# Performance work log

Measured on AMD Instinct MI355X. Metric: run time of the kernel, lower is better.

## Reference

```python
import jax, jax.numpy as jnp
import numpy as np

WS = 8          # window_size
SHIFT = 4       # shift_size
NUM_HEADS = 8
DIM = 256
HIDDEN = 1024   # mlp_ratio * dim
EPS = 1e-5


def _rel_pos_index(ws):
    # static numpy computation of Swin relative position index, shape (ws*ws, ws*ws)
    coords = np.stack(np.meshgrid(np.arange(ws), np.arange(ws), indexing='ij')).reshape(2, -1)
    rel = coords[:, :, None] - coords[:, None, :]            # (2, N, N)
    rel = rel.transpose(1, 2, 0).astype(np.int64)            # (N, N, 2)
    rel[..., 0] += ws - 1
    rel[..., 1] += ws - 1
    rel[..., 0] *= 2 * ws - 1
    return rel.sum(-1)                                       # (N, N)

_REL_IDX = _rel_pos_index(WS)


def _layer_norm(x, g, b):
    m = jnp.mean(x, axis=-1, keepdims=True)
    v = jnp.mean(jnp.square(x - m), axis=-1, keepdims=True)
    return (x - m) * jax.lax.rsqrt(v + EPS) * g + b


def _window_partition(x, ws):
    B, H, W, C = x.shape
    x = x.reshape(B, H // ws, ws, W // ws, ws, C)
    return x.transpose(0, 1, 3, 2, 4, 5).reshape(-1, ws * ws, C)


def _window_reverse(win, ws, B, H, W):
    C = win.shape[-1]
    x = win.reshape(B, H // ws, W // ws, ws, ws, C)
    return x.transpose(0, 1, 3, 2, 4, 5).reshape(B, H, W, C)


def setup_inputs() -> dict:
    key = jax.random.key(0)
    ks = jax.random.split(key, 16)
    s = 0.02
    inp = {
        'x': jax.random.normal(ks[0], (8, 16384, 256), jnp.float32),
        'norm1_w': jnp.ones((DIM,), jnp.float32),
        'norm1_b': jnp.zeros((DIM,), jnp.float32),
        'qkv_w': jax.random.normal(ks[1], (3 * DIM, DIM), jnp.float32) * s,
        'qkv_b': jnp.zeros((3 * DIM,), jnp.float32),
        'rpb_table': jax.random.normal(ks[2], ((2 * WS - 1) * (2 * WS - 1), NUM_HEADS), jnp.float32) * s,
        'proj_w': jax.random.normal(ks[3], (DIM, DIM), jnp.float32) * s,
        'proj_b': jnp.zeros((DIM,), jnp.float32),
        'norm2_w': jnp.ones((DIM,), jnp.float32),
        'norm2_b': jnp.zeros((DIM,), jnp.float32),
        'fc1_w': jax.random.normal(ks[4], (HIDDEN, DIM), jnp.float32) * s,
        'fc1_b': jnp.zeros((HIDDEN,), jnp.float32),
        'fc2_w': jax.random.normal(ks[5], (DIM, HIDDEN), jnp.float32) * s,
        'fc2_b': jnp.zeros((DIM,), jnp.float32),
        'h': 128,
        'w': 128,
    }
    return inp


def reference(x, norm1_w, norm1_b, qkv_w, qkv_b, rpb_table, proj_w, proj_b,
              norm2_w, norm2_b, fc1_w, fc1_b, fc2_w, fc2_b, h, w):
    B, L, C = x.shape
    H, W = int(h), int(w)
    nh, hd = NUM_HEADS, C // NUM_HEADS
    scale = hd ** -0.5
    N = WS * WS

    shortcut = x
    xn = _layer_norm(x, norm1_w, norm1_b).reshape(B, H, W, C)
    # cyclic shift (SW-MSA)
    xs = jnp.roll(xn, shift=(-SHIFT, -SHIFT), axis=(1, 2))
    xw = _window_partition(xs, WS)                           # (B_, N, C)

    # window attention
    qkv = xw @ qkv_w.T + qkv_b                               # (B_, N, 3C)
    qkv = qkv.reshape(-1, N, 3, nh, hd).transpose(2, 0, 3, 1, 4)
    q, k, v = qkv[0], qkv[1], qkv[2]                         # (B_, nh, N, hd)
    attn = jnp.einsum('bhnd,bhmd->bhnm', q * scale, k)
    bias = rpb_table[_REL_IDX.reshape(-1)].reshape(N, N, nh).transpose(2, 0, 1)
    attn = jax.nn.softmax(attn + bias[None], axis=-1)
    out = jnp.einsum('bhnm,bhmd->bhnd', attn, v)
    out = out.transpose(0, 2, 1, 3).reshape(-1, N, C)
    out = out @ proj_w.T + proj_b

    # merge windows and reverse shift
    xs = _window_reverse(out, WS, B, H, W)
    xo = jnp.roll(xs, shift=(SHIFT, SHIFT), axis=(1, 2)).reshape(B, H * W, C)

    x = shortcut + xo
    # MLP with residual
    y = _layer_norm(x, norm2_w, norm2_b)
    y = jax.nn.gelu(y @ fc1_w.T + fc1_b, approximate=False)
    y = y @ fc2_w.T + fc2_b
    return x + y
```

## Files before the change

### kernel.cpp

```cpp
#include <hip/hip_runtime.h>

typedef __bf16 bf16_t;
typedef __bf16 bf16x4 __attribute__((ext_vector_type(4)));
typedef __bf16 bf16x8 __attribute__((ext_vector_type(8)));
typedef float f32x4 __attribute__((ext_vector_type(4)));

#define QKV_SEG 33554432L

#define GLDS(gp, lp)                                                                   \
  __builtin_amdgcn_global_load_lds((const __attribute__((address_space(1))) void*)(gp), \
                                   (__attribute__((address_space(3))) void*)(lp), 16, 0, 0)
#define BAR __builtin_amdgcn_s_barrier()
#define SCHED0 __builtin_amdgcn_sched_barrier(0)
#define MFMA __builtin_amdgcn_mfma_f32_16x16x32_bf16

__global__ __launch_bounds__(256) void cvt_kernel(const float* __restrict__ src,
                                                  bf16_t* __restrict__ dst) {
  int i = (blockIdx.x * 256 + threadIdx.x) * 4;
  float4 v = *(const float4*)(src + i);
  bf16x4 o;
  o[0] = (bf16_t)v.x; o[1] = (bf16_t)v.y; o[2] = (bf16_t)v.z; o[3] = (bf16_t)v.w;
  *(bf16x4*)(dst + i) = o;
}

__global__ __launch_bounds__(256) void ln_kernel(const float* __restrict__ src,
                                                 const float* __restrict__ gw,
                                                 const float* __restrict__ gb,
                                                 bf16_t* __restrict__ dst,
                                                 int shifted) {
  int lane = threadIdx.x & 63, wv = threadIdx.x >> 6;
  long m = (long)blockIdx.x * 4 + wv;
  long srow;
  if (shifted) {
    long b_ = m >> 6; int tok = (int)(m & 63);
    int bb = (int)(b_ >> 8), win = (int)(b_ & 255);
    int wh = win >> 4, ww = win & 15;
    int ii = tok >> 3, jj = tok & 7;
    int hh = (wh * 8 + ii + 4) & 127, wp = (ww * 8 + jj + 4) & 127;
    srow = ((long)bb << 14) + (hh << 7) + wp;
  } else {
    srow = m;
  }
  float4 v = *(const float4*)(src + srow * 256 + lane * 4);
  float s = v.x + v.y + v.z + v.w;
  float s2 = v.x * v.x + v.y * v.y + v.z * v.z + v.w * v.w;
#pragma unroll
  for (int msk = 1; msk < 64; msk <<= 1) {
    s += __shfl_xor(s, msk);
    s2 += __shfl_xor(s2, msk);
  }
  float mean = s * (1.f / 256.f);
  float var = s2 * (1.f / 256.f) - mean * mean;
  float rs = rsqrtf(var + 1e-5f);
  float4 g4 = *(const float4*)(gw + lane * 4);
  float4 b4 = *(const float4*)(gb + lane * 4);
  bf16x4 o;
  o[0] = (bf16_t)((v.x - mean) * rs * g4.x + b4.x);
  o[1] = (bf16_t)((v.y - mean) * rs * g4.y + b4.y);
  o[2] = (bf16_t)((v.z - mean) * rs * g4.z + b4.z);
  o[3] = (bf16_t)((v.w - mean) * rs * g4.w + b4.w);
  *(bf16x4*)(dst + m * 256 + lane * 4) = o;
}

template <int EPI>
__global__ __launch_bounds__(256) void gemm_kernel(const bf16_t* __restrict__ A,
                                                   const bf16_t* __restrict__ Bw,
                                                   const float* __restrict__ bias, int K,
                                                   bf16_t* __restrict__ out_bf, float* out_f,
                                                   const float* resid) {
  __shared__ __align__(16) bf16_t As[2][8192];
  __shared__ __align__(16) bf16_t Bs[2][8192];
  int tid = threadIdx.x;
  int lane = tid & 63, wv = tid >> 6;
  int wm = wv >> 1, wn = wv & 1;

  int GX = gridDim.x, GY = gridDim.y;
  int flat = blockIdx.x + blockIdx.y * GX;
  int xcd = flat & 7, ii = flat >> 3;
  int iq = ii / GX;
  int by = xcd * (GY >> 3) + iq;
  int bx = ii - iq * GX;
  long m0 = (long)by * 128;
  int n0 = bx * 128;
  int lr = lane & 15, g = lane >> 4;

  int csw = (((lane & 7) ^ (lane >> 3)) << 3);
  const bf16_t* gA = A + (m0 + wv * 32 + (lane >> 3)) * K + csw;
  const bf16_t* gB = Bw + (long)(n0 + wv * 32 + (lane >> 3)) * K + csw;

  f32x4 acc[4][4] = {};

#define STAGE(buf, k0)                                                    \
  do {                                                                    \
    _Pragma("unroll") for (int s = 0; s < 4; ++s) {                       \
      GLDS(gA + (long)s * 8 * K + (k0), As[buf] + wv * 2048 + s * 512);   \
      GLDS(gB + (long)s * 8 * K + (k0), Bs[buf] + wv * 2048 + s * 512);   \
    }                                                                     \
  } while (0)

  int nt = K >> 6;
  STAGE(0, 0);
  for (int t = 0; t < nt; ++t) {
    int tb = t & 1;
    if (t + 1 < nt) {
      STAGE(tb ^ 1, (t + 1) << 6);
      asm volatile("s_waitcnt vmcnt(8)" ::: "memory");
    } else {
      asm volatile("s_waitcnt vmcnt(0)" ::: "memory");
    }
    BAR;
    SCHED0;
#pragma unroll
    for (int kk = 0; kk < 2; ++kk) {
      bf16x8 af[4], bfr[4];
#pragma unroll
      for (int mf = 0; mf < 4; ++mf)
        af[mf] = *(const bf16x8*)(As[tb] + (wm * 64 + mf * 16 + lr) * 64 +
                                  (((kk * 4 + g) ^ (lr & 7)) << 3));
#pragma unroll
      for (int nf = 0; nf < 4; ++nf)
        bfr[nf] = *(const bf16x8*)(Bs[tb] + (wn * 64 + nf * 16 + lr) * 64 +
                                   (((kk * 4 + g) ^ (lr & 7)) << 3));
#pragma unroll
      for (int mf = 0; mf < 4; ++mf)
#pragma unroll
        for (int nf = 0; nf < 4; ++nf)
          acc[mf][nf] = MFMA(af[mf], bfr[nf], acc[mf][nf], 0, 0, 0);
    }
    BAR;
  }
#undef STAGE

#pragma unroll
  for (int mf = 0; mf < 4; ++mf) {
#pragma unroll
    for (int nf = 0; nf < 4; ++nf) {
      long mb = m0 + wm * 64 + mf * 16 + 4 * g;
      int n = n0 + wn * 64 + nf * 16 + lr;
      float bn = bias[n];
      if (EPI == 0) {
        long b_ = mb >> 6;
        int tok = (int)(mb & 63);
        int which = n >> 8, rem = n & 255, head = rem >> 5, d = rem & 31;
        if (which == 2) {
          bf16x4 o;
#pragma unroll
          for (int r = 0; r < 4; ++r) o[r] = (bf16_t)(acc[mf][nf][r] + bn);
          *(bf16x4*)(out_bf + 2 * QKV_SEG + ((b_ * 8 + head) * 32 + d) * 64 + tok) = o;
        } else {
          long base = (long)which * QKV_SEG + ((b_ * 8 + head) * 64 + tok) * 32 + d;
#pragma unroll
          for (int r = 0; r < 4; ++r) out_bf[base + r * 32] = (bf16_t)(acc[mf][nf][r] + bn);
        }
      } else if (EPI == 1) {
#pragma unroll
        for (int r = 0; r < 4; ++r) {
          long m = mb + r;
          long b_ = m >> 6; int tok = (int)(m & 63);
          int bb = (int)(b_ >> 8), win = (int)(b_ & 255);
          int wh = win >> 4, ww = win & 15;
          int jj0 = tok >> 3, jj = tok & 7;
          int hh = (wh * 8 + jj0 + 4) & 127, wp = (ww * 8 + jj + 4) & 127;
          long dst = (((long)bb << 14) + (hh << 7) + wp) * 256 + n;
          out_f[dst] = acc[mf][nf][r] + bn + resid[dst];
        }
      }
    }
  }
}

__global__ __launch_bounds__(256, 3) void mlp_kernel(float* __restrict__ xio,
                                                     const float* __restrict__ gw,
                                                     const float* __restrict__ gb,
                                                     const bf16_t* __restrict__ w1,
                                                     const float* __restrict__ b1,
                                                     const bf16_t* __restrict__ w2,
                                                     const float* __restrict__ b2) {
  __shared__ __align__(16) bf16_t ys[64][264];
  __shared__ __align__(16) bf16_t hs[64][136];
  int tid = threadIdx.x, lane = tid & 63, wv = tid >> 6;
  long m0 = (long)blockIdx.x * 64;
  int lr = lane & 15, lk = (lane >> 4) * 8, g = lane >> 4;

  float4 g4 = *(const float4*)(gw + lane * 4);
  float4 b4 = *(const float4*)(gb + lane * 4);
#pragma unroll
  for (int i = 0; i < 16; ++i) {
    int r = wv * 16 + i;
    float4 v = *(const float4*)(xio + (m0 + r) * 256 + lane * 4);
    float s = v.x + v.y + v.z + v.w;
    float s2 = v.x * v.x + v.y * v.y + v.z * v.z + v.w * v.w;
#pragma unroll
    for (int msk = 1; msk < 64; msk <<= 1) {
      s += __shfl_xor(s, msk);
      s2 += __shfl_xor(s2, msk);
    }
    float mean = s * (1.f / 256.f);
    float var = s2 * (1.f / 256.f) - mean * mean;
    float rs = rsqrtf(var + 1e-5f);
    bf16x4 o;
    o[0] = (bf16_t)((v.x - mean) * rs * g4.x + b4.x);
    o[1] = (bf16_t)((v.y - mean) * rs * g4.y + b4.y);
    o[2] = (bf16_t)((v.z - mean) * rs * g4.z + b4.z);
    o[3] = (bf16_t)((v.w - mean) * rs * g4.w + b4.w);
    *(bf16x4*)(&ys[r][lane * 4]) = o;
  }
  __syncthreads();

  f32x4 acc2[4][4] = {};

  for (int hc = 0; hc < 8; ++hc) {
    f32x4 acc1[2][4] = {};
#pragma unroll
    for (int kk = 0; kk < 8; ++kk) {
      bf16x8 xf[2], yf[4];
#pragma unroll
      for (int mh = 0; mh < 2; ++mh)
        xf[mh] = *(const bf16x8*)(w1 + (long)(hc * 128 + wv * 32 + mh * 16 + lr) * 256 + kk * 32 + lk);
#pragma unroll
      for (int nt = 0; nt < 4; ++nt)
        yf[nt] = *(const bf16x8*)(&ys[nt * 16 + lr][kk * 32 + lk]);
#pragma unroll
      for (int mh = 0; mh < 2; ++mh)
#pragma unroll
        for (int nt = 0; nt < 4; ++nt)
          acc1[mh][nt] = MFMA(xf[mh], yf[nt], acc1[mh][nt], 0, 0, 0);
    }
#pragma unroll
    for (int mh = 0; mh < 2; ++mh) {
      float4 bb = *(const float4*)(b1 + hc * 128 + wv * 32 + mh * 16 + 4 * g);
#pragma unroll
      for (int nt = 0; nt < 4; ++nt) {
        bf16x4 o;
#pragma unroll
        for (int r = 0; r < 4; ++r) {
          float val = acc1[mh][nt][r] + ((const float*)&bb)[r];
          o[r] = (bf16_t)(0.5f * val * (1.0f + erff(val * 0.70710678118654752f)));
        }
        *(bf16x4*)(&hs[nt * 16 + lr][wv * 32 + mh * 16 + 4 * g]) = o;
      }
    }
    __syncthreads();
#pragma unroll
    for (int kk = 0; kk < 4; ++kk) {
      bf16x8 ah[4], bw[4];
#pragma unroll
      for (int mf = 0; mf < 4; ++mf)
        ah[mf] = *(const bf16x8*)(&hs[mf * 16 + lr][kk * 32 + lk]);
#pragma unroll
      for (int nf = 0; nf < 4; ++nf)
        bw[nf] = *(const bf16x8*)(w2 + (long)(wv * 64 + nf * 16 + lr) * 1024 + hc * 128 + kk * 32 + lk);
#pragma unroll
      for (int mf = 0; mf < 4; ++mf)
#pragma unroll
        for (int nf = 0; nf < 4; ++nf)
          acc2[mf][nf] = MFMA(ah[mf], bw[nf], acc2[mf][nf], 0, 0, 0);
    }
    __syncthreads();
  }

#pragma unroll
  for (int mf = 0; mf < 4; ++mf)
#pragma unroll
    for (int nf = 0; nf < 4; ++nf) {
      float bn = b2[wv * 64 + nf * 16 + lr];
#pragma unroll
      for (int r = 0; r < 4; ++r) {
        long idx = (m0 + mf * 16 + 4 * g + r) * 256 + wv * 64 + nf * 16 + lr;
        xio[idx] = acc2[mf][nf][r] + bn + xio[idx];
      }
    }
}

__global__ __launch_bounds__(256) void attn_kernel(const bf16_t* __restrict__ qkv,
                                                   const float* __restrict__ rpb,
                                                   bf16_t* __restrict__ attn_out) {
  __shared__ float rpb_s[1800];
  __shared__ bf16_t P[4][64][72];
  int tid = threadIdx.x, lane = tid & 63, wv = tid >> 6;
  long b_ = blockIdx.x;
  for (int i = tid; i < 1800; i += 256) rpb_s[i] = rpb[i];
  __syncthreads();
  const bf16_t* q = qkv;
  const bf16_t* k = qkv + QKV_SEG;
  const bf16_t* vt = qkv + 2 * QKV_SEG;
  int lr = lane & 15, lk = (lane >> 4) * 8, g = lane >> 4;
  const float scale = 0.17677669529663688f;

  for (int hh = 0; hh < 2; ++hh) {
    int head = wv * 2 + hh;
    long base = (b_ * 8 + head) * 2048;
    bf16x8 af[4], bfr[4];
#pragma unroll
    for (int mf = 0; mf < 4; ++mf)
      af[mf] = *(const bf16x8*)(q + base + (mf * 16 + lr) * 32 + lk);
#pragma unroll
    for (int nf = 0; nf < 4; ++nf)
      bfr[nf] = *(const bf16x8*)(k + base + (nf * 16 + lr) * 32 + lk);
    f32x4 S[4][4] = {};
#pragma unroll
    for (int mf = 0; mf < 4; ++mf)
#pragma unroll
      for (int nf = 0; nf < 4; ++nf)
        S[mf][nf] = MFMA(af[mf], bfr[nf], S[mf][nf], 0, 0, 0);
#pragma unroll
    for (int mf = 0; mf < 4; ++mf)
#pragma unroll
      for (int nf = 0; nf < 4; ++nf)
#pragma unroll
        for (int r = 0; r < 4; ++r) {
          int i = mf * 16 + 4 * g + r, j = nf * 16 + lr;
          int rel = ((i >> 3) - (j >> 3) + 7) * 15 + ((i & 7) - (j & 7) + 7);
          S[mf][nf][r] = S[mf][nf][r] * scale + rpb_s[rel * 8 + head];
        }
#pragma unroll
    for (int mf = 0; mf < 4; ++mf) {
#pragma unroll
      for (int r = 0; r < 4; ++r) {
        float mx = fmaxf(fmaxf(S[mf][0][r], S[mf][1][r]), fmaxf(S[mf][2][r], S[mf][3][r]));
#pragma unroll
        for (int msk = 1; msk < 16; msk <<= 1) mx = fmaxf(mx, __shfl_xor(mx, msk));
        float sm = 0.f;
#pragma unroll
        for (int nf = 0; nf < 4; ++nf) {
          float e = __expf(S[mf][nf][r] - mx);
          S[mf][nf][r] = e;
          sm += e;
        }
#pragma unroll
        for (int msk = 1; msk < 16; msk <<= 1) sm += __shfl_xor(sm, msk);
        float is = 1.f / sm;
        int i = mf * 16 + 4 * g + r;
#pragma unroll
        for (int nf = 0; nf < 4; ++nf) P[wv][i][nf * 16 + lr] = (bf16_t)(S[mf][nf][r] * is);
      }
    }
    f32x4 O[4][2] = {};
#pragma unroll
    for (int ks = 0; ks < 2; ++ks) {
      int j0 = ks * 32;
      bf16x8 pa[4], vb[2];
#pragma unroll
      for (int mf = 0; mf < 4; ++mf) pa[mf] = *(const bf16x8*)(&P[wv][mf * 16 + lr][j0 + lk]);
#pragma unroll
      for (int nf = 0; nf < 2; ++nf)
        vb[nf] = *(const bf16x8*)(vt + base + (nf * 16 + lr) * 64 + j0 + lk);
#pragma unroll
      for (int mf = 0; mf < 4; ++mf)
#pragma unroll
        for (int nf = 0; nf < 2; ++nf)
          O[mf][nf] = MFMA(pa[mf], vb[nf], O[mf][nf], 0, 0, 0);
    }
#pragma unroll
    for (int mf = 0; mf < 4; ++mf)
#pragma unroll
      for (int nf = 0; nf < 2; ++nf)
#pragma unroll
        for (int r = 0; r < 4; ++r) {
          int i = mf * 16 + 4 * g + r, d = nf * 16 + lr;
          attn_out[(b_ * 64 + i) * 256 + head * 32 + d] = (bf16_t)O[mf][nf][r];
        }
  }
}

extern "C" void kernel_launch(void* const* d_in, const int* in_sizes, int n_in,
                              void* d_out, int out_size, void* d_ws, size_t ws_size,
                              hipStream_t stream) {
  const float* x = (const float*)d_in[0];
  const float* n1w = (const float*)d_in[1];
  const float* n1b = (const float*)d_in[2];
  const float* qkv_w = (const float*)d_in[3];
  const float* qkv_b = (const float*)d_in[4];
  const float* rpb = (const float*)d_in[5];
  const float* proj_w = (const float*)d_in[6];
  const float* proj_b = (const float*)d_in[7];
  const float* n2w = (const float*)d_in[8];
  const float* n2b = (const float*)d_in[9];
  const float* fc1_w = (const float*)d_in[10];
  const float* fc1_b = (const float*)d_in[11];
  const float* fc2_w = (const float*)d_in[12];
  const float* fc2_b = (const float*)d_in[13];
  float* out = (float*)d_out;

  char* ws = (char*)d_ws;
  bf16_t* bufA = (bf16_t*)ws;
  bf16_t* bufB = (bf16_t*)(ws + 268435456L);
  bf16_t* wq = (bf16_t*)(ws + 335544320L);
  bf16_t* wp = wq + 196608;
  bf16_t* w1 = wp + 65536;
  bf16_t* w2 = w1 + 262144;

  cvt_kernel<<<192, 256, 0, stream>>>(qkv_w, wq);
  cvt_kernel<<<64, 256, 0, stream>>>(proj_w, wp);
  cvt_kernel<<<256, 256, 0, stream>>>(fc1_w, w1);
  cvt_kernel<<<256, 256, 0, stream>>>(fc2_w, w2);

  ln_kernel<<<32768, 256, 0, stream>>>(x, n1w, n1b, bufB, 1);
  gemm_kernel<0><<<dim3(6, 1024), 256, 0, stream>>>(bufB, wq, qkv_b, 256, bufA, nullptr, nullptr);
  attn_kernel<<<2048, 256, 0, stream>>>(bufA, rpb, bufB);
  gemm_kernel<1><<<dim3(2, 1024), 256, 0, stream>>>(bufB, wp, proj_b, 256, nullptr, out, x);
  mlp_kernel<<<2048, 256, 0, stream>>>(out, n2w, n2b, w1, fc1_b, w2, fc2_b);
}
```

Baseline: 746.6 us.

## Store residual in bf16 and retile MLP to 32-row blocks with swizzled LDS

The projection GEMM now writes the post-attention residual sum as bf16 into a workspace buffer instead of fp32. The MLP kernel reads that bf16 tensor and writes the final fp32 output separately. The MLP block shrinks from 64 to 32 rows (twice the blocks, occupancy hint 4). Its LDS tiles drop padding for an XOR swizzle, and double-buffering the hidden tile removes one barrier per chunk. This aims to cut memory traffic and raise occupancy, but the residual stream is rounded to bf16, costing accuracy, and each block now reloads weights for half as many rows.

```diff
diff --git a/kernel.cpp b/kernel.cpp
--- a/kernel.cpp
+++ b/kernel.cpp
@@ -26,21 +26,16 @@
 __global__ __launch_bounds__(256) void ln_kernel(const float* __restrict__ src,
                                                  const float* __restrict__ gw,
                                                  const float* __restrict__ gb,
-                                                 bf16_t* __restrict__ dst,
-                                                 int shifted) {
+                                                 bf16_t* __restrict__ dst) {
   int lane = threadIdx.x & 63, wv = threadIdx.x >> 6;
   long m = (long)blockIdx.x * 4 + wv;
-  long srow;
-  if (shifted) {
-    long b_ = m >> 6; int tok = (int)(m & 63);
-    int bb = (int)(b_ >> 8), win = (int)(b_ & 255);
-    int wh = win >> 4, ww = win & 15;
-    int ii = tok >> 3, jj = tok & 7;
-    int hh = (wh * 8 + ii + 4) & 127, wp = (ww * 8 + jj + 4) & 127;
-    srow = ((long)bb << 14) + (hh << 7) + wp;
-  } else {
-    srow = m;
-  }
+  long b_ = m >> 6; int tok = (int)(m & 63);
+  int bb = (int)(b_ >> 8), win = (int)(b_ & 255);
+  int wh = win >> 4, ww = win & 15;
+  int ii = tok >> 3, jj = tok & 7;
+  int hh = (wh * 8 + ii + 4) & 127, wp = (ww * 8 + jj + 4) & 127;
+  long srow = ((long)bb << 14) + (hh << 7) + wp;
+
   float4 v = *(const float4*)(src + srow * 256 + lane * 4);
   float s = v.x + v.y + v.z + v.w;
   float s2 = v.x * v.x + v.y * v.y + v.z * v.z + v.w * v.w;
@@ -66,7 +61,7 @@
 __global__ __launch_bounds__(256) void gemm_kernel(const bf16_t* __restrict__ A,
                                                    const bf16_t* __restrict__ Bw,
                                                    const float* __restrict__ bias, int K,
-                                                   bf16_t* __restrict__ out_bf, float* out_f,
+                                                   bf16_t* __restrict__ out_bf,
                                                    const float* resid) {
   __shared__ __align__(16) bf16_t As[2][8192];
   __shared__ __align__(16) bf16_t Bs[2][8192];
@@ -152,7 +147,7 @@
 #pragma unroll
           for (int r = 0; r < 4; ++r) out_bf[base + r * 32] = (bf16_t)(acc[mf][nf][r] + bn);
         }
-      } else if (EPI == 1) {
+      } else {
 #pragma unroll
         for (int r = 0; r < 4; ++r) {
           long m = mb + r;
@@ -162,34 +157,36 @@
           int jj0 = tok >> 3, jj = tok & 7;
           int hh = (wh * 8 + jj0 + 4) & 127, wp = (ww * 8 + jj + 4) & 127;
           long dst = (((long)bb << 14) + (hh << 7) + wp) * 256 + n;
-          out_f[dst] = acc[mf][nf][r] + bn + resid[dst];
+          out_bf[dst] = (bf16_t)(acc[mf][nf][r] + bn + resid[dst]);
         }
       }
     }
   }
 }
 
-__global__ __launch_bounds__(256, 3) void mlp_kernel(float* __restrict__ xio,
+__global__ __launch_bounds__(256, 4) void mlp_kernel(const bf16_t* __restrict__ x1b,
+                                                     float* __restrict__ out,
                                                      const float* __restrict__ gw,
                                                      const float* __restrict__ gb,
                                                      const bf16_t* __restrict__ w1,
                                                      const float* __restrict__ b1,
                                                      const bf16_t* __restrict__ w2,
                                                      const float* __restrict__ b2) {
-  __shared__ __align__(16) bf16_t ys[64][264];
-  __shared__ __align__(16) bf16_t hs[64][136];
+  __shared__ __align__(16) bf16_t ys[32 * 256];
+  __shared__ __align__(16) bf16_t hs[2][32 * 128];
   int tid = threadIdx.x, lane = tid & 63, wv = tid >> 6;
-  long m0 = (long)blockIdx.x * 64;
+  long m0 = (long)blockIdx.x * 32;
   int lr = lane & 15, lk = (lane >> 4) * 8, g = lane >> 4;
 
   float4 g4 = *(const float4*)(gw + lane * 4);
   float4 b4 = *(const float4*)(gb + lane * 4);
 #pragma unroll
-  for (int i = 0; i < 16; ++i) {
-    int r = wv * 16 + i;
-    float4 v = *(const float4*)(xio + (m0 + r) * 256 + lane * 4);
-    float s = v.x + v.y + v.z + v.w;
-    float s2 = v.x * v.x + v.y * v.y + v.z * v.z + v.w * v.w;
+  for (int i = 0; i < 8; ++i) {
+    int r = wv * 8 + i;
+    bf16x4 xv = *(const bf16x4*)(x1b + (m0 + r) * 256 + lane * 4);
+    float v0 = (float)xv[0], v1 = (float)xv[1], v2 = (float)xv[2], v3 = (float)xv[3];
+    float s = v0 + v1 + v2 + v3;
+    float s2 = v0 * v0 + v1 * v1 + v2 * v2 + v3 * v3;
 #pragma unroll
     for (int msk = 1; msk < 64; msk <<= 1) {
       s += __shfl_xor(s, msk);
@@ -199,75 +196,77 @@
     float var = s2 * (1.f / 256.f) - mean * mean;
     float rs = rsqrtf(var + 1e-5f);
     bf16x4 o;
-    o[0] = (bf16_t)((v.x - mean) * rs * g4.x + b4.x);
-    o[1] = (bf16_t)((v.y - mean) * rs * g4.y + b4.y);
-    o[2] = (bf16_t)((v.z - mean) * rs * g4.z + b4.z);
-    o[3] = (bf16_t)((v.w - mean) * rs * g4.w + b4.w);
-    *(bf16x4*)(&ys[r][lane * 4]) = o;
+    o[0] = (bf16_t)((v0 - mean) * rs * g4.x + b4.x);
+    o[1] = (bf16_t)((v1 - mean) * rs * g4.y + b4.y);
+    o[2] = (bf16_t)((v2 - mean) * rs * g4.z + b4.z);
+    o[3] = (bf16_t)((v3 - mean) * rs * g4.w + b4.w);
+    *(bf16x4*)(ys + r * 256 + ((((lane >> 1) ^ (r & 7)) << 3) | ((lane & 1) << 2))) = o;
   }
   __syncthreads();
 
-  f32x4 acc2[4][4] = {};
+  f32x4 acc2[2][4] = {};
 
   for (int hc = 0; hc < 8; ++hc) {
-    f32x4 acc1[2][4] = {};
+    int p = hc & 1;
+    f32x4 acc1[2][2] = {};
 #pragma unroll
     for (int kk = 0; kk < 8; ++kk) {
-      bf16x8 xf[2], yf[4];
+      bf16x8 xf[2], yf[2];
 #pragma unroll
       for (int mh = 0; mh < 2; ++mh)
         xf[mh] = *(const bf16x8*)(w1 + (long)(hc * 128 + wv * 32 + mh * 16 + lr) * 256 + kk * 32 + lk);
 #pragma unroll
-      for (int nt = 0; nt < 4; ++nt)
-        yf[nt] = *(const bf16x8*)(&ys[nt * 16 + lr][kk * 32 + lk]);
+      for (int nt = 0; nt < 2; ++nt)
+        yf[nt] = *(const bf16x8*)(ys + (nt * 16 + lr) * 256 + (((kk * 4 + g) ^ (lr & 7)) << 3));
 #pragma unroll
       for (int mh = 0; mh < 2; ++mh)
 #pragma unroll
-        for (int nt = 0; nt < 4; ++nt)
+        for (int nt = 0; nt < 2; ++nt)
           acc1[mh][nt] = MFMA(xf[mh], yf[nt], acc1[mh][nt], 0, 0, 0);
     }
 #pragma unroll
     for (int mh = 0; mh < 2; ++mh) {
       float4 bb = *(const float4*)(b1 + hc * 128 + wv * 32 + mh * 16 + 4 * g);
 #pragma unroll
-      for (int nt = 0; nt < 4; ++nt) {
+      for (int nt = 0; nt < 2; ++nt) {
         bf16x4 o;
 #pragma unroll
         for (int r = 0; r < 4; ++r) {
           float val = acc1[mh][nt][r] + ((const float*)&bb)[r];
           o[r] = (bf16_t)(0.5f * val * (1.0f + erff(val * 0.70710678118654752f)));
         }
-        *(bf16x4*)(&hs[nt * 16 + lr][wv * 32 + mh * 16 + 4 * g]) = o;
+        int chunk = (wv * 4 + mh * 2 + (g >> 1)) ^ (lr & 7);
+        *(bf16x4*)(hs[p] + (nt * 16 + lr) * 128 + (chunk << 3) + ((g & 1) << 2)) = o;
       }
     }
     __syncthreads();
 #pragma unroll
     for (int kk = 0; kk < 4; ++kk) {
-      bf16x8 ah[4], bw[4];
-#pragma unroll
-      for (int mf = 0; mf < 4; ++mf)
-        ah[mf] = *(const bf16x8*)(&hs[mf * 16 + lr][kk * 32 + lk]);
+      bf16x8 ah[2], bw[4];
+#pragma unroll
+      for (int mf = 0; mf < 2; ++mf)
+        ah[mf] = *(const bf16x8*)(hs[p] + (mf * 16 + lr) * 128 + (((kk * 4 + g) ^ (lr & 7)) << 3));
 #pragma unroll
       for (int nf = 0; nf < 4; ++nf)
         bw[nf] = *(const bf16x8*)(w2 + (long)(wv * 64 + nf * 16 + lr) * 1024 + hc * 128 + kk * 32 + lk);
 #pragma unroll
-      for (int mf = 0; mf < 4; ++mf)
+      for (int mf = 0; mf < 2; ++mf)
 #pragma unroll
         for (int nf = 0; nf < 4; ++nf)
           acc2[mf][nf] = MFMA(ah[mf], bw[nf], acc2[mf][nf], 0, 0, 0);
     }
-    __syncthreads();
-  }
-
-#pragma unroll
-  for (int mf = 0; mf < 4; ++mf)
+  }
+
+#pragma unroll
+  for (int mf = 0; mf < 2; ++mf)
 #pragma unroll
     for (int nf = 0; nf < 4; ++nf) {
-      float bn = b2[wv * 64 + nf * 16 + lr];
+      int n = wv * 64 + nf * 16 + lr;
+      float bn = b2[n];
 #pragma unroll
       for (int r = 0; r < 4; ++r) {
-        long idx = (m0 + mf * 16 + 4 * g + r) * 256 + wv * 64 + nf * 16 + lr;
-        xio[idx] = acc2[mf][nf][r] + bn + xio[idx];
+        long row = m0 + mf * 16 + 4 * g + r;
+        out[row * 256 + n] = acc2[mf][nf][r] + bn + (float)x1b[row * 256 + n];
       }
     }
 }
@@ -384,6 +383,7 @@
 
   char* ws = (char*)d_ws;
   bf16_t* bufA = (bf16_t*)ws;
+  bf16_t* x1b = (bf16_t*)(ws + 201326592L);
   bf16_t* bufB = (bf16_t*)(ws + 268435456L);
   bf16_t* wq = (bf16_t*)(ws + 335544320L);
   bf16_t* wp = wq + 196608;
@@ -395,9 +395,9 @@
   cvt_kernel<<<256, 256, 0, stream>>>(fc1_w, w1);
   cvt_kernel<<<256, 256, 0, stream>>>(fc2_w, w2);
 
-  ln_kernel<<<32768, 256, 0, stream>>>(x, n1w, n1b, bufB, 1);
-  gemm_kernel<0><<<dim3(6, 1024), 256, 0, stream>>>(bufB, wq, qkv_b, 256, bufA, nullptr, nullptr);
+  ln_kernel<<<32768, 256, 0, stream>>>(x, n1w, n1b, bufB);
+  gemm_kernel<0><<<dim3(6, 1024), 256, 0, stream>>>(bufB, wq, qkv_b, 256, bufA, nullptr);
   attn_kernel<<<2048, 256, 0, stream>>>(bufA, rpb, bufB);
-  gemm_kernel<1><<<dim3(2, 1024), 256, 0, stream>>>(bufB, wp, proj_b, 256, nullptr, out, x);
-  mlp_kernel<<<2048, 256, 0, stream>>>(out, n2w, n2b, w1, fc1_b, w2, fc2_b);
-}
+  gemm_kernel<1><<<dim3(2, 1024), 256, 0, stream>>>(bufB, wp, proj_b, 256, x1b, x);
+  mlp_kernel<<<4096, 256, 0, stream>>>(x1b, out, n2w, n2b, w1, fc1_b, w2, fc2_b);
+}
```

Result: slower. 794.1 us (+6.4%).
